# Kernel tuning notes

Hardware: AMD Instinct MI355X
Metric: run time of the kernel (lower is better)

Reference implementation:

```python
import jax, jax.numpy as jnp
import numpy as np

LOG2 = float(np.log(2.0))

def ssp(x):
    # shifted softplus, the PhysNet-family activation: softplus(x) - ln(2)
    return jax.nn.softplus(x) - LOG2

def setup_inputs() -> dict:
    key = jax.random.key(0)
    k1, k2, k3, k4, k5 = jax.random.split(key, 5)
    N, E, D_EDGE, D_RBF = 50000, 640000, 128, 64
    vi = jax.random.normal(k1, (N, D_EDGE), dtype=jnp.float32)
    rbf = jax.random.uniform(k2, (E, D_RBF), dtype=jnp.float32)
    edge_index = jax.random.randint(k3, (2, E), 0, N, dtype=jnp.int64)
    # torch.nn.Linear params: y = x @ W.T + b, W ~ U(-1/sqrt(fan_in), 1/sqrt(fan_in))
    s1 = 1.0 / np.sqrt(D_RBF)
    s2 = 1.0 / np.sqrt(3 * D_EDGE)
    W_rbf = jax.random.uniform(k4, (D_EDGE, D_RBF), jnp.float32, -s1, s1)
    b_rbf = jnp.zeros((D_EDGE,), jnp.float32)
    W_cat = jax.random.uniform(k5, (D_EDGE, 3 * D_EDGE), jnp.float32, -s2, s2)
    b_cat = jnp.zeros((D_EDGE,), jnp.float32)
    return {"vi": vi, "rbf": rbf, "W_rbf": W_rbf, "b_rbf": b_rbf,
            "W_cat": W_cat, "b_cat": b_cat, "edge_index": edge_index}

def reference(vi, rbf, W_rbf, b_rbf, W_cat, b_cat, edge_index):
    # gather endpoint features per edge: [E, D]
    h_i = vi[edge_index[0], :]
    h_j = vi[edge_index[1], :]
    rbf_proj = rbf @ W_rbf.T + b_rbf              # [E, D]
    concat_msg = jnp.concatenate([rbf_proj, h_j, h_i], axis=-1)  # [E, 3D]
    m_ji = ssp(concat_msg @ W_cat.T + b_cat)      # [E, D]
    return m_ji
```

## Files before the change

### kernel.cpp

```cpp
#include <hip/hip_runtime.h>
#include <cmath>

#define D  128
#define DR 64
#define NB 32

typedef float fx4    __attribute__((ext_vector_type(4)));
typedef float f32x16 __attribute__((ext_vector_type(16)));
typedef short short8v __attribute__((ext_vector_type(8)));

__device__ __forceinline__ float ssp_f(float x) {
  float m = fmaxf(x, 0.0f);
  float t = __expf(-fabsf(x));
  return m + __logf(1.0f + t) - 0.69314718055994531f;
}

__device__ __forceinline__ short f2bf(float f) {
  unsigned u = __float_as_uint(f);
  u = (u + 0x7FFFu + ((u >> 16) & 1u)) >> 16;
  return (short)u;
}

__global__ __launch_bounds__(256) void stage0_kernel(
    const float* __restrict__ W_rbf, const float* __restrict__ b_rbf,
    const float* __restrict__ W_cat, const float* __restrict__ b_cat,
    float* __restrict__ weff, unsigned short* __restrict__ weffh,
    float* __restrict__ beff, int write_bf16)
{
  int gid = blockIdx.x * 256 + threadIdx.x;
  if (gid < D * DR) {
    int o = gid >> 6;
    int r = gid & 63;
    float acc = 0.0f;
    #pragma unroll 8
    for (int d = 0; d < D; ++d)
      acc = fmaf(W_cat[o * 384 + d], W_rbf[d * DR + r], acc);
    weff[gid] = acc;
    if (write_bf16) weffh[gid] = (unsigned short)f2bf(acc);
  }
  if (gid < D) {
    float acc = b_cat[gid];
    #pragma unroll 8
    for (int d = 0; d < D; ++d)
      acc = fmaf(b_rbf[d], W_cat[gid * 384 + d], acc);
    beff[gid] = acc;
  }
}

__global__ __launch_bounds__(256) void stage1_kernel(
    const float* __restrict__ vi, const float* __restrict__ W_cat,
    float* __restrict__ Pj, float* __restrict__ Pi, int N)
{
  __shared__ float vrow[NB * D];
  int base = blockIdx.x * NB;
  int t = threadIdx.x;
  for (int idx = t * 4; idx < NB * D; idx += 1024) {
    int n = base + (idx >> 7);
    float4 v = make_float4(0.f, 0.f, 0.f, 0.f);
    if (n < N) v = *(const float4*)&vi[(long)n * D + (idx & 127)];
    *(float4*)&vrow[idx] = v;
  }
  __syncthreads();

  int o     = t & 127;
  int which = t >> 7;
  const float* w = W_cat + (long)o * 384 + 128 + which * 128;
  float* P = which ? Pi : Pj;

  float acc[NB];
  #pragma unroll
  for (int n = 0; n < NB; ++n) acc[n] = 0.0f;

  for (int dd = 0; dd < D; dd += 4) {
    float4 wv = *(const float4*)&w[dd];
    #pragma unroll
    for (int n = 0; n < NB; ++n) {
      float4 v = *(const float4*)&vrow[n * D + dd];
      acc[n] = fmaf(wv.x, v.x, acc[n]);
      acc[n] = fmaf(wv.y, v.y, acc[n]);
      acc[n] = fmaf(wv.z, v.z, acc[n]);
      acc[n] = fmaf(wv.w, v.w, acc[n]);
    }
  }
  #pragma unroll
  for (int n = 0; n < NB; ++n) {
    int nn = base + n;
    if (nn < N) P[(long)nn * D + o] = acc[n];
  }
}

__global__ __launch_bounds__(256) void edge_mfma_kernel(
    const float* __restrict__ rbf, const int* __restrict__ eidx,
    const unsigned short* __restrict__ weffh, const float* __restrict__ beff,
    const float* __restrict__ Pj, const float* __restrict__ Pi,
    float* __restrict__ out, int E)
{
  const int t    = threadIdx.x;
  const int lane = t & 63;
  const int row  = lane & 31;
  const int half = lane >> 5;
  const long wid  = (long)blockIdx.x * 4 + (t >> 6);
  const long base = wid * 64;
  if (base >= (long)E) return;

  short8v B[4][4];
  #pragma unroll
  for (int ct = 0; ct < 4; ++ct) {
    #pragma unroll
    for (int ks = 0; ks < 4; ++ks)
      B[ct][ks] = *(const short8v*)&weffh[(ct * 32 + row) * DR + ks * 16 + half * 8];
  }
  float bias[4];
  #pragma unroll
  for (int ct = 0; ct < 4; ++ct) bias[ct] = beff[ct * 32 + row];

  #pragma unroll
  for (int tile = 0; tile < 2; ++tile) {
    const long tb = base + (long)tile * 32;
    if (tb >= (long)E) break;
    long er = tb + row; if (er > (long)E - 1) er = (long)E - 1;

    const float* arow = rbf + er * DR + half * 8;
    short8v A[4];
    #pragma unroll
    for (int ks = 0; ks < 4; ++ks) {
      fx4 lo = *(const fx4*)&arow[ks * 16];
      fx4 hi = *(const fx4*)&arow[ks * 16 + 4];
      short8v a;
      a[0] = f2bf(lo.x); a[1] = f2bf(lo.y); a[2] = f2bf(lo.z); a[3] = f2bf(lo.w);
      a[4] = f2bf(hi.x); a[5] = f2bf(hi.y); a[6] = f2bf(hi.z); a[7] = f2bf(hi.w);
      A[ks] = a;
    }

    const int iv = eidx[er];
    const int jv = eidx[(long)E + er];

    #pragma unroll
    for (int ct = 0; ct < 4; ++ct) {
      float gj[16], gi[16];
      #pragma unroll
      for (int reg = 0; reg < 16; ++reg) {
        const int erl = (reg & 3) + 8 * (reg >> 2) + 4 * half;
        const int j = __shfl(jv, erl);
        const int i = __shfl(iv, erl);
        gj[reg] = Pj[(long)j * D + ct * 32 + row];
        gi[reg] = Pi[(long)i * D + ct * 32 + row];
      }
      __builtin_amdgcn_sched_barrier(0);

      f32x16 acc = (f32x16)(0.0f);
      acc = __builtin_amdgcn_mfma_f32_32x32x16_bf16(A[0], B[ct][0], acc, 0, 0, 0);
      acc = __builtin_amdgcn_mfma_f32_32x32x16_bf16(A[1], B[ct][1], acc, 0, 0, 0);
      acc = __builtin_amdgcn_mfma_f32_32x32x16_bf16(A[2], B[ct][2], acc, 0, 0, 0);
      acc = __builtin_amdgcn_mfma_f32_32x32x16_bf16(A[3], B[ct][3], acc, 0, 0, 0);

      #pragma unroll
      for (int reg = 0; reg < 16; ++reg) {
        const int erl = (reg & 3) + 8 * (reg >> 2) + 4 * half;
        const long ge = tb + erl;
        const float v = ssp_f(acc[reg] + gj[reg] + gi[reg] + bias[ct]);
        if (ge < (long)E) out[ge * D + ct * 32 + row] = v;
      }
    }
  }
}

template<int K, int WS, int WOFF, bool GATHER, bool INIT, bool FINAL>
__global__ __launch_bounds__(256) void pass_kernel(
    const float* __restrict__ src, const int* __restrict__ gidx,
    const float* __restrict__ W, const float* __restrict__ beff,
    float* __restrict__ out, int E)
{
  int e = blockIdx.x * 256 + threadIdx.x;
  if (e >= E) return;
  long rowi = GATHER ? (long)gidx[e] : (long)e;

  float4 rv[K / 4];
  const float4* sp = (const float4*)(src + rowi * K);
  #pragma unroll
  for (int c = 0; c < K / 4; ++c) rv[c] = sp[c];

  float* orow = out + (long)e * D;
  for (int ob = 0; ob < D; ob += 4) {
    float acc[4];
    if (INIT) {
      float4 b4 = *(const float4*)&beff[ob];
      acc[0] = b4.x; acc[1] = b4.y; acc[2] = b4.z; acc[3] = b4.w;
    } else {
      float4 p4 = *(const float4*)&orow[ob];
      acc[0] = p4.x; acc[1] = p4.y; acc[2] = p4.z; acc[3] = p4.w;
    }
    #pragma unroll
    for (int k = 0; k < 4; ++k) {
      const float4* wv = (const float4*)&W[(long)(ob + k) * WS + WOFF];
      float a = acc[k];
      #pragma unroll
      for (int c = 0; c < K / 4; ++c) {
        float4 w4 = wv[c]; float4 r4 = rv[c];
        a = fmaf(w4.x, r4.x, a); a = fmaf(w4.y, r4.y, a);
        a = fmaf(w4.z, r4.z, a); a = fmaf(w4.w, r4.w, a);
      }
      acc[k] = a;
    }
    float4 o4;
    o4.x = FINAL ? ssp_f(acc[0]) : acc[0];
    o4.y = FINAL ? ssp_f(acc[1]) : acc[1];
    o4.z = FINAL ? ssp_f(acc[2]) : acc[2];
    o4.w = FINAL ? ssp_f(acc[3]) : acc[3];
    *(float4*)&orow[ob] = o4;
  }
}

extern "C" void kernel_launch(void* const* d_in, const int* in_sizes, int n_in,
                              void* d_out, int out_size, void* d_ws, size_t ws_size,
                              hipStream_t stream)
{
  const float* vi    = (const float*)d_in[0];
  const float* rbf   = (const float*)d_in[1];
  const float* W_rbf = (const float*)d_in[2];
  const float* b_rbf = (const float*)d_in[3];
  const float* W_cat = (const float*)d_in[4];
  const float* b_cat = (const float*)d_in[5];
  const int*   eidx  = (const int*)d_in[6];

  const int N = in_sizes[0] / D;
  const int E = in_sizes[6] / 2;
  float* out = (float*)d_out;

  float* ws   = (float*)d_ws;
  float* weff = ws;
  float* beff = ws + D * DR;
  unsigned short* weffh = (unsigned short*)(ws + 8448);
  float* Pj   = ws + 8448 + 4096;
  float* Pi   = Pj + (size_t)N * D;
  size_t need = (8448 + 4096 + 2 * (size_t)N * D) * sizeof(float);

  const int use_fast = (ws_size >= need && E >= 1);
  stage0_kernel<<<32, 256, 0, stream>>>(W_rbf, b_rbf, W_cat, b_cat,
                                        weff, weffh, beff, use_fast);

  if (use_fast) {
    stage1_kernel<<<(N + NB - 1) / NB, 256, 0, stream>>>(vi, W_cat, Pj, Pi, N);
    long waves = ((long)E + 63) / 64;
    int fblocks = (int)((waves + 3) / 4);
    edge_mfma_kernel<<<fblocks, 256, 0, stream>>>(rbf, eidx, weffh, beff,
                                                  Pj, Pi, out, E);
  } else {
    int eblocks = (E + 255) / 256;
    pass_kernel<DR, DR, 0,  false, true,  false><<<eblocks, 256, 0, stream>>>(rbf, nullptr,  weff,  beff, out, E);
    pass_kernel<D, 384, 128, true, false, false><<<eblocks, 256, 0, stream>>>(vi,  eidx + E, W_cat, beff, out, E);
    pass_kernel<D, 384, 256, true, false, true ><<<eblocks, 256, 0, stream>>>(vi,  eidx,     W_cat, beff, out, E);
  }
}
```

Baseline: 287.1 us.

## Software-pipeline gathers across column tiles and halve edges per wave in edge kernel

The edge kernel now handles 32 edges per wave instead of 64, doubling the grid. It double-buffers the Pj/Pi gathers and weight fragments so that the loads for the next column tile are issued before the MFMA and epilogue of the current one. It also precomputes byte offsets for the gathers, folds the bias into the accumulator init, and uses nontemporal loads for rbf and nontemporal stores for the output. The aim is to hide gather latency and avoid polluting the cache with streaming data, at the cost of more registers and reloading B per wave.

```diff
diff --git a/kernel.cpp b/kernel.cpp
--- a/kernel.cpp
+++ b/kernel.cpp
@@ -99,70 +99,104 @@
   const int lane = t & 63;
   const int row  = lane & 31;
   const int half = lane >> 5;
-  const long wid  = (long)blockIdx.x * 4 + (t >> 6);
-  const long base = wid * 64;
-  if (base >= (long)E) return;
-
-  short8v B[4][4];
-  #pragma unroll
-  for (int ct = 0; ct < 4; ++ct) {
-    #pragma unroll
-    for (int ks = 0; ks < 4; ++ks)
-      B[ct][ks] = *(const short8v*)&weffh[(ct * 32 + row) * DR + ks * 16 + half * 8];
-  }
-  float bias[4];
-  #pragma unroll
-  for (int ct = 0; ct < 4; ++ct) bias[ct] = beff[ct * 32 + row];
-
-  #pragma unroll
-  for (int tile = 0; tile < 2; ++tile) {
-    const long tb = base + (long)tile * 32;
-    if (tb >= (long)E) break;
-    long er = tb + row; if (er > (long)E - 1) er = (long)E - 1;
-
-    const float* arow = rbf + er * DR + half * 8;
-    short8v A[4];
-    #pragma unroll
-    for (int ks = 0; ks < 4; ++ks) {
-      fx4 lo = *(const fx4*)&arow[ks * 16];
-      fx4 hi = *(const fx4*)&arow[ks * 16 + 4];
-      short8v a;
-      a[0] = f2bf(lo.x); a[1] = f2bf(lo.y); a[2] = f2bf(lo.z); a[3] = f2bf(lo.w);
-      a[4] = f2bf(hi.x); a[5] = f2bf(hi.y); a[6] = f2bf(hi.z); a[7] = f2bf(hi.w);
-      A[ks] = a;
-    }
-
-    const int iv = eidx[er];
-    const int jv = eidx[(long)E + er];
-
-    #pragma unroll
-    for (int ct = 0; ct < 4; ++ct) {
-      float gj[16], gi[16];
-      #pragma unroll
-      for (int reg = 0; reg < 16; ++reg) {
-        const int erl = (reg & 3) + 8 * (reg >> 2) + 4 * half;
-        const int j = __shfl(jv, erl);
-        const int i = __shfl(iv, erl);
-        gj[reg] = Pj[(long)j * D + ct * 32 + row];
-        gi[reg] = Pi[(long)i * D + ct * 32 + row];
-      }
-      __builtin_amdgcn_sched_barrier(0);
-
-      f32x16 acc = (f32x16)(0.0f);
-      acc = __builtin_amdgcn_mfma_f32_32x32x16_bf16(A[0], B[ct][0], acc, 0, 0, 0);
-      acc = __builtin_amdgcn_mfma_f32_32x32x16_bf16(A[1], B[ct][1], acc, 0, 0, 0);
-      acc = __builtin_amdgcn_mfma_f32_32x32x16_bf16(A[2], B[ct][2], acc, 0, 0, 0);
-      acc = __builtin_amdgcn_mfma_f32_32x32x16_bf16(A[3], B[ct][3], acc, 0, 0, 0);
-
-      #pragma unroll
-      for (int reg = 0; reg < 16; ++reg) {
-        const int erl = (reg & 3) + 8 * (reg >> 2) + 4 * half;
-        const long ge = tb + erl;
-        const float v = ssp_f(acc[reg] + gj[reg] + gi[reg] + bias[ct]);
-        if (ge < (long)E) out[ge * D + ct * 32 + row] = v;
-      }
-    }
-  }
+  const long wid = (long)blockIdx.x * 4 + (t >> 6);
+  const long tb  = wid * 32;
+  if (tb >= (long)E) return;
+
+  const char* PjB = (const char*)Pj;
+  const char* PiB = (const char*)Pi;
+
+  int jb[16], ib[16];
+  #pragma unroll
+  for (int reg = 0; reg < 16; ++reg) {
+    const int erl = (reg & 3) + 8 * (reg >> 2) + 4 * half;
+    long eg = tb + erl; if (eg > (long)E - 1) eg = (long)E - 1;
+    jb[reg] = eidx[(long)E + eg];
+    ib[reg] = eidx[eg];
+  }
+  #pragma unroll
+  for (int reg = 0; reg < 16; ++reg) {
+    jb[reg] = (jb[reg] << 9) + row * 4;
+    ib[reg] = (ib[reg] << 9) + row * 4;
+  }
+
+  long er = tb + row; if (er > (long)E - 1) er = (long)E - 1;
+  const float* arow = rbf + er * DR + half * 8;
+  short8v A[4];
+  #pragma unroll
+  for (int ks = 0; ks < 4; ++ks) {
+    fx4 lo = __builtin_nontemporal_load((const fx4*)&arow[ks * 16]);
+    fx4 hi = __builtin_nontemporal_load((const fx4*)&arow[ks * 16 + 4]);
+    short8v a;
+    a[0] = f2bf(lo.x); a[1] = f2bf(lo.y); a[2] = f2bf(lo.z); a[3] = f2bf(lo.w);
+    a[4] = f2bf(hi.x); a[5] = f2bf(hi.y); a[6] = f2bf(hi.z); a[7] = f2bf(hi.w);
+    A[ks] = a;
+  }
+
+#define LOAD_B(Bv, biasv, ct)                                                  \
+  { _Pragma("unroll")                                                          \
+    for (int ks = 0; ks < 4; ++ks)                                             \
+      Bv[ks] = *(const short8v*)&weffh[((ct) * 32 + row) * DR + ks * 16 + half * 8]; \
+    biasv = beff[(ct) * 32 + row]; }
+
+#define ISSUE_G(gjv, giv, ct)                                                  \
+  { _Pragma("unroll")                                                          \
+    for (int reg = 0; reg < 16; ++reg) {                                       \
+      gjv[reg] = *(const float*)(PjB + (long)jb[reg] + (ct) * 128);            \
+      giv[reg] = *(const float*)(PiB + (long)ib[reg] + (ct) * 128);            \
+    } }
+
+#define MFMA4(accv, Bv, biasv)                                                 \
+  { _Pragma("unroll")                                                          \
+    for (int i = 0; i < 16; ++i) accv[i] = biasv;                              \
+    accv = __builtin_amdgcn_mfma_f32_32x32x16_bf16(A[0], Bv[0], accv, 0, 0, 0);\
+    accv = __builtin_amdgcn_mfma_f32_32x32x16_bf16(A[1], Bv[1], accv, 0, 0, 0);\
+    accv = __builtin_amdgcn_mfma_f32_32x32x16_bf16(A[2], Bv[2], accv, 0, 0, 0);\
+    accv = __builtin_amdgcn_mfma_f32_32x32x16_bf16(A[3], Bv[3], accv, 0, 0, 0); }
+
+#define EPILOG(gjv, giv, accv, ct)                                             \
+  { _Pragma("unroll")                                                          \
+    for (int reg = 0; reg < 16; ++reg) {                                       \
+      const int erl = (reg & 3) + 8 * (reg >> 2) + 4 * half;                   \
+      const long ge = tb + erl;                                                \
+      const float v = ssp_f(accv[reg] + gjv[reg] + giv[reg]);                  \
+      if (ge < (long)E)                                                        \
+        __builtin_nontemporal_store(v, &out[ge * D + (ct) * 32 + row]);        \
+    } }
+
+  float gjA[16], giA[16], gjB[16], giB[16];
+  short8v BA[4], BB[4];
+  float biasA, biasB;
+  f32x16 acc;
+
+  LOAD_B(BA, biasA, 0);
+  ISSUE_G(gjA, giA, 0);
+
+  LOAD_B(BB, biasB, 1);
+  ISSUE_G(gjB, giB, 1);
+  __builtin_amdgcn_sched_barrier(0);
+  MFMA4(acc, BA, biasA);
+  EPILOG(gjA, giA, acc, 0);
+
+  LOAD_B(BA, biasA, 2);
+  ISSUE_G(gjA, giA, 2);
+  __builtin_amdgcn_sched_barrier(0);
+  MFMA4(acc, BB, biasB);
+  EPILOG(gjB, giB, acc, 1);
+
+  LOAD_B(BB, biasB, 3);
+  ISSUE_G(gjB, giB, 3);
+  __builtin_amdgcn_sched_barrier(0);
+  MFMA4(acc, BA, biasA);
+  EPILOG(gjA, giA, acc, 2);
+
+  MFMA4(acc, BB, biasB);
+  EPILOG(gjB, giB, acc, 3);
+
+#undef LOAD_B
+#undef ISSUE_G
+#undef MFMA4
+#undef EPILOG
 }
 
 template<int K, int WS, int WOFF, bool GATHER, bool INIT, bool FINAL>
@@ -241,7 +275,7 @@
 
   if (use_fast) {
     stage1_kernel<<<(N + NB - 1) / NB, 256, 0, stream>>>(vi, W_cat, Pj, Pi, N);
-    long waves = ((long)E + 63) / 64;
+    long waves = ((long)E + 31) / 32;
     int fblocks = (int)((waves + 3) / 4);
     edge_mfma_kernel<<<fblocks, 256, 0, stream>>>(rbf, eidx, weffh, beff,
                                                   Pj, Pi, out, E);
```

New measurement: 325.7 us. 1.13x slower.

## Restructure edge kernel to 16x16x32 MFMA tiles of 16 edges per wave

Applied to the files above, without the earlier changes.

The edge kernel now gives each wave 16 edges instead of 64 and uses the 16x16x32 bf16 MFMA in place of 32x32x16. Weight fragments are loaded per column tile from global memory rather than held in registers, and the bias seeds the accumulator. rbf is read with nontemporal loads, and gather/store offsets are precomputed as 32-bit byte offsets, which is why a bound on N is added. The intent is to cut register pressure and raise occupancy and memory parallelism for the gather-heavy, bandwidth-bound edge pass, at the cost of more launched waves and repeated weight loads.

```diff
diff --git a/kernel.cpp b/kernel.cpp
--- a/kernel.cpp
+++ b/kernel.cpp
@@ -6,7 +6,6 @@
 #define NB 32
 
 typedef float fx4    __attribute__((ext_vector_type(4)));
-typedef float f32x16 __attribute__((ext_vector_type(16)));
 typedef short short8v __attribute__((ext_vector_type(8)));
 
 __device__ __forceinline__ float ssp_f(float x) {
@@ -97,70 +96,62 @@
 {
   const int t    = threadIdx.x;
   const int lane = t & 63;
-  const int row  = lane & 31;
-  const int half = lane >> 5;
-  const long wid  = (long)blockIdx.x * 4 + (t >> 6);
-  const long base = wid * 64;
-  if (base >= (long)E) return;
-
-  short8v B[4][4];
-  #pragma unroll
-  for (int ct = 0; ct < 4; ++ct) {
-    #pragma unroll
-    for (int ks = 0; ks < 4; ++ks)
-      B[ct][ks] = *(const short8v*)&weffh[(ct * 32 + row) * DR + ks * 16 + half * 8];
-  }
-  float bias[4];
-  #pragma unroll
-  for (int ct = 0; ct < 4; ++ct) bias[ct] = beff[ct * 32 + row];
-
-  #pragma unroll
-  for (int tile = 0; tile < 2; ++tile) {
-    const long tb = base + (long)tile * 32;
-    if (tb >= (long)E) break;
-    long er = tb + row; if (er > (long)E - 1) er = (long)E - 1;
-
-    const float* arow = rbf + er * DR + half * 8;
-    short8v A[4];
-    #pragma unroll
-    for (int ks = 0; ks < 4; ++ks) {
-      fx4 lo = *(const fx4*)&arow[ks * 16];
-      fx4 hi = *(const fx4*)&arow[ks * 16 + 4];
-      short8v a;
-      a[0] = f2bf(lo.x); a[1] = f2bf(lo.y); a[2] = f2bf(lo.z); a[3] = f2bf(lo.w);
-      a[4] = f2bf(hi.x); a[5] = f2bf(hi.y); a[6] = f2bf(hi.z); a[7] = f2bf(hi.w);
-      A[ks] = a;
-    }
-
-    const int iv = eidx[er];
-    const int jv = eidx[(long)E + er];
-
-    #pragma unroll
-    for (int ct = 0; ct < 4; ++ct) {
-      float gj[16], gi[16];
-      #pragma unroll
-      for (int reg = 0; reg < 16; ++reg) {
-        const int erl = (reg & 3) + 8 * (reg >> 2) + 4 * half;
-        const int j = __shfl(jv, erl);
-        const int i = __shfl(iv, erl);
-        gj[reg] = Pj[(long)j * D + ct * 32 + row];
-        gi[reg] = Pi[(long)i * D + ct * 32 + row];
-      }
-      __builtin_amdgcn_sched_barrier(0);
-
-      f32x16 acc = (f32x16)(0.0f);
-      acc = __builtin_amdgcn_mfma_f32_32x32x16_bf16(A[0], B[ct][0], acc, 0, 0, 0);
-      acc = __builtin_amdgcn_mfma_f32_32x32x16_bf16(A[1], B[ct][1], acc, 0, 0, 0);
-      acc = __builtin_amdgcn_mfma_f32_32x32x16_bf16(A[2], B[ct][2], acc, 0, 0, 0);
-      acc = __builtin_amdgcn_mfma_f32_32x32x16_bf16(A[3], B[ct][3], acc, 0, 0, 0);
-
-      #pragma unroll
-      for (int reg = 0; reg < 16; ++reg) {
-        const int erl = (reg & 3) + 8 * (reg >> 2) + 4 * half;
-        const long ge = tb + erl;
-        const float v = ssp_f(acc[reg] + gj[reg] + gi[reg] + bias[ct]);
-        if (ge < (long)E) out[ge * D + ct * 32 + row] = v;
-      }
+  const int n16  = lane & 15;
+  const int kg   = lane >> 4;
+  const long wid = (long)blockIdx.x * 4 + (t >> 6);
+  const long tb  = wid * 16;
+  if (tb >= (long)E) return;
+
+  long ar = tb + n16; if (ar > (long)E - 1) ar = (long)E - 1;
+  const float* arow = rbf + ar * DR + kg * 8;
+  short8v A0, A1;
+  {
+    fx4 l0 = __builtin_nontemporal_load((const fx4*)&arow[0]);
+    fx4 h0 = __builtin_nontemporal_load((const fx4*)&arow[4]);
+    fx4 l1 = __builtin_nontemporal_load((const fx4*)&arow[32]);
+    fx4 h1 = __builtin_nontemporal_load((const fx4*)&arow[36]);
+    A0[0] = f2bf(l0.x); A0[1] = f2bf(l0.y); A0[2] = f2bf(l0.z); A0[3] = f2bf(l0.w);
+    A0[4] = f2bf(h0.x); A0[5] = f2bf(h0.y); A0[6] = f2bf(h0.z); A0[7] = f2bf(h0.w);
+    A1[0] = f2bf(l1.x); A1[1] = f2bf(l1.y); A1[2] = f2bf(l1.z); A1[3] = f2bf(l1.w);
+    A1[4] = f2bf(h1.x); A1[5] = f2bf(h1.y); A1[6] = f2bf(h1.z); A1[7] = f2bf(h1.w);
+  }
+
+  int joff[4], ioff[4], soff[4];
+  bool ok[4];
+  #pragma unroll
+  for (int reg = 0; reg < 4; ++reg) {
+    const long ge = tb + kg * 4 + reg;
+    ok[reg] = ge < (long)E;
+    const long gc = ok[reg] ? ge : (long)E - 1;
+    joff[reg] = eidx[(long)E + gc] * 512 + n16 * 4;
+    ioff[reg] = eidx[gc] * 512 + n16 * 4;
+    soff[reg] = (int)(ge * 512) + n16 * 4;
+  }
+
+  const char* PjB = (const char*)Pj;
+  const char* PiB = (const char*)Pi;
+  char* outB = (char*)out;
+
+  #pragma unroll
+  for (int ct = 0; ct < 8; ++ct) {
+    short8v B0 = *(const short8v*)&weffh[(ct * 16 + n16) * DR + kg * 8];
+    short8v B1 = *(const short8v*)&weffh[(ct * 16 + n16) * DR + 32 + kg * 8];
+    float gj[4], gi[4];
+    #pragma unroll
+    for (int reg = 0; reg < 4; ++reg) {
+      gj[reg] = *(const float*)(PjB + (long)joff[reg] + ct * 64);
+      gi[reg] = *(const float*)(PiB + (long)ioff[reg] + ct * 64);
+    }
+    const float bias = beff[ct * 16 + n16];
+
+    fx4 acc = {bias, bias, bias, bias};
+    acc = __builtin_amdgcn_mfma_f32_16x16x32_bf16(A0, B0, acc, 0, 0, 0);
+    acc = __builtin_amdgcn_mfma_f32_16x16x32_bf16(A1, B1, acc, 0, 0, 0);
+
+    #pragma unroll
+    for (int reg = 0; reg < 4; ++reg) {
+      const float v = ssp_f(acc[reg] + gj[reg] + gi[reg]);
+      if (ok[reg]) *(float*)(outB + (long)soff[reg] + ct * 64) = v;
     }
   }
 }
@@ -235,14 +226,13 @@
   float* Pi   = Pj + (size_t)N * D;
   size_t need = (8448 + 4096 + 2 * (size_t)N * D) * sizeof(float);
 
-  const int use_fast = (ws_size >= need && E >= 1);
+  const int use_fast = (ws_size >= need && E >= 1 && N < 4000000);
   stage0_kernel<<<32, 256, 0, stream>>>(W_rbf, b_rbf, W_cat, b_cat,
                                         weff, weffh, beff, use_fast);
 
   if (use_fast) {
     stage1_kernel<<<(N + NB - 1) / NB, 256, 0, stream>>>(vi, W_cat, Pj, Pi, N);
-    long waves = ((long)E + 63) / 64;
-    int fblocks = (int)((waves + 3) / 4);
+    int fblocks = (int)(((long)E + 63) / 64);
     edge_mfma_kernel<<<fblocks, 256, 0, stream>>>(rbf, eidx, weffh, beff,
                                                   Pj, Pi, out, E);
   } else {
```

Result: slower. 347.7 us (+21.1%).
